# Performance work log

Measured on AMD Instinct MI355X. Metric: run time of the kernel, lower is better.

The kernel has to match this reference:

```python
import jax, jax.numpy as jnp
import numpy as np

B, C, N = 4, 256, 4096
OUT = 256
TEMP = OUT ** 0.5  # temperature = sqrt(out_channel)


def setup_inputs() -> dict:
    key = jax.random.key(0)
    kx, kxx, kq, kk, kv = jax.random.split(key, 5)
    x = jax.random.normal(kx, (B, C, N), dtype=jnp.float32)
    xx = jax.random.normal(kxx, (B, C, N), dtype=jnp.float32)
    # Conv1d(in, out, kernel=1, bias=False) weights, squeezed to (out, in)
    s = 1.0 / np.sqrt(C)
    Wq = jax.random.uniform(kq, (OUT, C), jnp.float32, -s, s)
    Wk = jax.random.uniform(kk, (OUT, C), jnp.float32, -s, s)
    Wv = jax.random.uniform(kv, (OUT, C), jnp.float32, -s, s)
    return {"x": x, "xx": xx, "Wq": Wq, "Wk": Wk, "Wv": Wv}


def reference(x, xx, Wq, Wk, Wv):
    # 1x1 conv == per-point linear: (out,in) x (b,in,n) -> (b,out,n)
    q = jnp.einsum('oc,bcn->bon', Wq, x)
    k = jnp.einsum('oc,bcn->bon', Wk, xx)
    v = jnp.einsum('oc,bcn->bon', Wv, xx)
    # attn = (q^T / temp) @ k : (B, N, N)
    attn = jax.nn.softmax(jnp.einsum('bon,bom->bnm', q, k) / TEMP, axis=-1)
    # dropout is identity in eval mode
    # y = attn @ v^T -> (B, N, OUT); returned transposed to (B, OUT, N)
    y = jnp.einsum('bnm,bom->bon', attn, v)
    return y
```

## Files before the change

kernel.cpp:

```cpp
#include <hip/hip_runtime.h>
#include <hip/hip_bf16.h>


typedef __attribute__((ext_vector_type(8))) short bf16x8;
typedef __attribute__((ext_vector_type(4))) float f32x4;
typedef __attribute__((ext_vector_type(4))) short short4t;

constexpr int B_ = 4;
constexpr int C_ = 256;
constexpr int N_ = 4096;
constexpr int O_ = 256;
constexpr float INV_TEMP = 1.0f / 16.0f;
constexpr int SPLIT = 4;
constexpr int MCHUNK = N_ / SPLIT;
constexpr int NITER = MCHUNK / 32;

__device__ __forceinline__ short f2bf(float f) {
  union { float f; unsigned u; } v; v.f = f;
  unsigned r = v.u + 0x7fffu + ((v.u >> 16) & 1u);
  return (short)(r >> 16);
}

__device__ __forceinline__ void dma16(const short* g, short* l) {
  __builtin_amdgcn_global_load_lds(
      (const __attribute__((address_space(1))) unsigned int*)g,
      (__attribute__((address_space(3))) unsigned int*)l, 16, 0, 0);
}

__global__ void wcvt(const float* __restrict__ Wq, const float* __restrict__ Wk,
                     const float* __restrict__ Wv, short* __restrict__ wb) {
  int i = blockIdx.x * 256 + threadIdx.x;
  int mat = i >> 16, off = i & 65535;
  const float* W = (mat == 0) ? Wq : (mat == 1 ? Wk : Wv);
  wb[i] = f2bf(W[off]);
}

__global__ void zero_k(float4* __restrict__ out4, float4* __restrict__ lp4) {
  int i = blockIdx.x * 256 + threadIdx.x;
  if (i < 1048576) out4[i] = (float4){0.f, 0.f, 0.f, 0.f};
  else lp4[i - 1048576] = (float4){0.f, 0.f, 0.f, 0.f};
}

__global__ void norm_k(float* __restrict__ out, const float* __restrict__ lp) {
  int i = blockIdx.x * 256 + threadIdx.x;
  int e = i * 4;
  int n = e & (N_ - 1);
  int b = e >> 20;
  float4 o = ((float4*)out)[i];
  const float4 l = *(const float4*)&lp[(b << 12) + n];
  o.x /= l.x; o.y /= l.y; o.z /= l.z; o.w /= l.w;
  ((float4*)out)[i] = o;
}

__device__ __forceinline__ void gemm64(const short* __restrict__ W,
                                       const short (*xs)[264], int w, int g,
                                       int c16, f32x4 acc[4][4]) {
#pragma unroll
  for (int i = 0; i < 4; ++i)
#pragma unroll
    for (int j = 0; j < 4; ++j) acc[i][j] = (f32x4){0.f, 0.f, 0.f, 0.f};
#pragma unroll
  for (int ko = 0; ko < 8; ++ko) {
    bf16x8 afr[4], bfr[4];
#pragma unroll
    for (int ot = 0; ot < 4; ++ot)
      afr[ot] = *(const bf16x8*)&W[(w * 64 + ot * 16 + c16) * C_ + ko * 32 + g * 8];
#pragma unroll
    for (int nt = 0; nt < 4; ++nt)
      bfr[nt] = *(const bf16x8*)&xs[nt * 16 + c16][ko * 32 + g * 8];
#pragma unroll
    for (int ot = 0; ot < 4; ++ot)
#pragma unroll
      for (int nt = 0; nt < 4; ++nt)
        acc[ot][nt] = __builtin_amdgcn_mfma_f32_16x16x32_bf16(
            afr[ot], bfr[nt], acc[ot][nt], 0, 0, 0);
  }
}

__global__ __launch_bounds__(256, 2) void qkv_proj(
    const float* __restrict__ x, const float* __restrict__ xx,
    const short* __restrict__ wb,
    short* __restrict__ qg, short* __restrict__ kt, short* __restrict__ vt) {
  const int n0  = blockIdx.x * 64;
  const int b   = blockIdx.y;
  const int mat = blockIdx.z;
  const float* src = (mat == 0) ? x : xx;
  const int tid = threadIdx.x;
  const int w = tid >> 6, lane = tid & 63;
  const int g = lane >> 4, c16 = lane & 15;

  __shared__ short xs[64][264];

  {
    const int n = tid & 63, cq = tid >> 6;
    const float* sp = src + (size_t)b * C_ * N_ + n0 + n;
#pragma unroll
    for (int rep = 0; rep < 16; ++rep) {
      int c = rep * 16 + cq * 4;
      short4t s4;
#pragma unroll
      for (int j = 0; j < 4; ++j) s4[j] = f2bf(sp[(size_t)(c + j) * N_]);
      *(short4t*)&xs[n][c] = s4;
    }
  }
  __syncthreads();

  f32x4 acc[4][4];
  if (mat == 0) {
    gemm64(wb, &xs[0], w, g, c16, acc);
    short* dst = qg + (size_t)b * N_ * O_;
#pragma unroll
    for (int ot = 0; ot < 4; ++ot)
#pragma unroll
      for (int nt = 0; nt < 4; ++nt) {
        int n = n0 + nt * 16 + c16;
        int o = w * 64 + ot * 16 + g * 4;
        short4t s;
        s[0] = f2bf(acc[ot][nt][0] * INV_TEMP);
        s[1] = f2bf(acc[ot][nt][1] * INV_TEMP);
        s[2] = f2bf(acc[ot][nt][2] * INV_TEMP);
        s[3] = f2bf(acc[ot][nt][3] * INV_TEMP);
        *(short4t*)(dst + (size_t)n * O_ + o) = s;
      }
  } else {
    gemm64(wb + 65536, &xs[0], w, g, c16, acc);
#pragma unroll
    for (int ot = 0; ot < 4; ++ot)
#pragma unroll
      for (int nt = 0; nt < 4; ++nt) {
        int m = n0 + nt * 16 + c16;
        int o0 = w * 64 + ot * 16 + g * 4;
        int koo = o0 >> 5;
        int pos = ((o0 & 31) >> 3) ^ ((c16 >> 1) & 3);
        size_t base =
            (((size_t)(b * 256 + (m >> 4)) * 8 + koo) * 16 + c16) * 32 +
            pos * 8 + (g & 1) * 4;
        short4t s;
        s[0] = f2bf(acc[ot][nt][0]);
        s[1] = f2bf(acc[ot][nt][1]);
        s[2] = f2bf(acc[ot][nt][2]);
        s[3] = f2bf(acc[ot][nt][3]);
        *(short4t*)(kt + base) = s;
      }
    gemm64(wb + 131072, &xs[0], w, g, c16, acc);
#pragma unroll
    for (int ot = 0; ot < 4; ++ot)
#pragma unroll
      for (int nt = 0; nt < 4; ++nt) {
        int m = n0 + nt * 16 + c16;
        size_t rowb = (size_t)(b * 128 + (m >> 5)) * 256;
        int gqm = (m & 31) >> 3, e = m & 7;
        int o0 = w * 64 + ot * 16 + g * 4;
#pragma unroll
        for (int r = 0; r < 4; ++r) {
          int o = o0 + r;
          int pos = gqm ^ (((o & 15) >> 1) & 3);
          vt[(rowb + o) * 32 + pos * 8 + e] = f2bf(acc[ot][nt][r]);
        }
      }
  }
}

__global__ __launch_bounds__(256, 2) void flash_attn(
    const short* __restrict__ qg, const short* __restrict__ kt,
    const short* __restrict__ vt, float* __restrict__ out,
    float* __restrict__ lp) {
  const int n0 = blockIdx.x * 128;
  const int b  = blockIdx.y;
  const int mbase = blockIdx.z * MCHUNK;
  const int tid = threadIdx.x;
  const int w = tid >> 6, lane = tid & 63;
  const int g = lane >> 4, c16 = lane & 15;

  __shared__ short kb[2][8192];
  __shared__ short vb[8192];
  __shared__ short ps[128][40];

  const short* ktb = kt + (size_t)b * N_ * O_;
  const short* vtb = vt + (size_t)b * N_ * O_;

  bf16x8 qf[2][8];
#pragma unroll
  for (int nt = 0; nt < 2; ++nt) {
    const short* qrow =
        qg + (size_t)(b * N_ + n0 + w * 32 + nt * 16 + c16) * O_ + g * 8;
#pragma unroll
    for (int ko = 0; ko < 8; ++ko) qf[nt][ko] = *(const bf16x8*)(qrow + ko * 32);
  }

  f32x4 oacc[16][2];
#pragma unroll
  for (int i = 0; i < 16; ++i)
#pragma unroll
    for (int nt = 0; nt < 2; ++nt) oacc[i][nt] = (f32x4){0.f, 0.f, 0.f, 0.f};
  float lrun[2] = {0.f, 0.f};

  {
    const short* src = ktb + (size_t)(mbase >> 4) * 4096;
#pragma unroll
    for (int j = 0; j < 4; ++j)
      dma16(src + (w * 4 + j) * 512 + lane * 8, &kb[0][(w * 4 + j) * 512]);
  }
  __syncthreads();

  const int sw = (g ^ ((c16 >> 1) & 3)) * 8;

  int cur = 0;
  for (int mi = 0; mi < NITER; ++mi) {
    {
      const short* src = vtb + ((size_t)(mbase >> 5) + mi) * 8192;
#pragma unroll
      for (int j = 0; j < 4; ++j)
        dma16(src + (w * 4 + j) * 512 + lane * 8, &vb[(w * 4 + j) * 512]);
    }
    if (mi + 1 < NITER) {
      const short* src = ktb + (size_t)((mbase >> 4) + (mi + 1) * 2) * 4096;
#pragma unroll
      for (int j = 0; j < 4; ++j)
        dma16(src + (w * 4 + j) * 512 + lane * 8, &kb[cur ^ 1][(w * 4 + j) * 512]);
    }

    f32x4 sacc[2][2];
#pragma unroll
    for (int nt = 0; nt < 2; ++nt)
#pragma unroll
      for (int t2 = 0; t2 < 2; ++t2) sacc[nt][t2] = (f32x4){0.f, 0.f, 0.f, 0.f};
#pragma unroll
    for (int ko = 0; ko < 8; ++ko) {
      const int ra = (ko * 16 + c16) * 32 + sw;
      bf16x8 kfa = *(const bf16x8*)&kb[cur][ra];
      bf16x8 kfb = *(const bf16x8*)&kb[cur][4096 + ra];
#pragma unroll
      for (int nt = 0; nt < 2; ++nt) {
        sacc[nt][0] = __builtin_amdgcn_mfma_f32_16x16x32_bf16(
            kfa, qf[nt][ko], sacc[nt][0], 0, 0, 0);
        sacc[nt][1] = __builtin_amdgcn_mfma_f32_16x16x32_bf16(
            kfb, qf[nt][ko], sacc[nt][1], 0, 0, 0);
      }
    }

#pragma unroll
    for (int nt = 0; nt < 2; ++nt) {
      float rs = 0.f;
#pragma unroll
      for (int t2 = 0; t2 < 2; ++t2) {
        short4t pb;
#pragma unroll
        for (int r = 0; r < 4; ++r) {
          float p = __expf(sacc[nt][t2][r]);
          rs += p;
          pb[r] = f2bf(p);
        }
        *(short4t*)&ps[w * 32 + nt * 16 + c16][t2 * 16 + g * 4] = pb;
      }
      rs += __shfl_xor(rs, 16);
      rs += __shfl_xor(rs, 32);
      lrun[nt] += rs;
    }

    __syncthreads();

    bf16x8 pf[2];
#pragma unroll
    for (int nt = 0; nt < 2; ++nt)
      pf[nt] = *(const bf16x8*)&ps[w * 32 + nt * 16 + c16][g * 8];
#pragma unroll
    for (int ot = 0; ot < 16; ++ot) {
      bf16x8 vf = *(const bf16x8*)&vb[(ot * 16 + c16) * 32 + sw];
#pragma unroll
      for (int nt = 0; nt < 2; ++nt)
        oacc[ot][nt] = __builtin_amdgcn_mfma_f32_16x16x32_bf16(
            vf, pf[nt], oacc[ot][nt], 0, 0, 0);
    }

    __syncthreads();
    cur ^= 1;
  }

  if (g == 0)
#pragma unroll
    for (int nt = 0; nt < 2; ++nt)
      atomicAdd(&lp[(b << 12) + n0 + w * 32 + nt * 16 + c16], lrun[nt]);

#pragma unroll
  for (int ot = 0; ot < 16; ++ot)
#pragma unroll
    for (int nt = 0; nt < 2; ++nt) {
      const int n = n0 + w * 32 + nt * 16 + c16;
      float* op = out + (size_t)b * O_ * N_ + (size_t)(ot * 16 + g * 4) * N_ + n;
#pragma unroll
      for (int r = 0; r < 4; ++r)
        atomicAdd(op + (size_t)r * N_, oacc[ot][nt][r]);
    }
}

extern "C" void kernel_launch(void* const* d_in, const int* in_sizes, int n_in,
                              void* d_out, int out_size, void* d_ws,
                              size_t ws_size, hipStream_t stream) {
  const float* x  = (const float*)d_in[0];
  const float* xx = (const float*)d_in[1];
  const float* Wq = (const float*)d_in[2];
  const float* Wk = (const float*)d_in[3];
  const float* Wv = (const float*)d_in[4];
  float* out = (float*)d_out;

  short* qg = (short*)d_ws;
  short* kt = qg + (size_t)B_ * N_ * O_;
  short* vt = kt + (size_t)B_ * N_ * O_;
  float* lp = (float*)(vt + (size_t)B_ * N_ * O_);
  short* wb = (short*)(lp + B_ * N_);

  wcvt<<<768, 256, 0, stream>>>(Wq, Wk, Wv, wb);
  zero_k<<<4112, 256, 0, stream>>>((float4*)out, (float4*)lp);
  qkv_proj<<<dim3(N_ / 64, B_, 2), 256, 0, stream>>>(x, xx, wb, qg, kt, vt);
  flash_attn<<<dim3(32, B_, SPLIT), 256, 0, stream>>>(qg, kt, vt, out, lp);
  norm_k<<<4096, 256, 0, stream>>>(out, lp);
}
```

Baseline: 219.9 us.

## Retile flash attention to 64-query blocks with 64-key steps and per-wave output slices

Reworks the attention kernel so each block handles 64 queries and 64 keys per iteration. Each wave computes scores for its own 16-key slice and owns a 64-channel slice of the output instead of all 256 channels. The key-split count drops from 4 to 2 and the grid doubles along queries, so fewer atomic partial outputs are written. The K double buffer is replaced by a single buffer whose prefetch is issued after a barrier, and V gets a new swizzled 64-wide layout written with vector stores. The projection kernel now runs Q, K and V as three separate grid slices with a transposed MFMA for V. The single K buffer can expose load latency, and the block count changes occupancy.

```diff
diff --git a/kernel.cpp b/kernel.cpp
--- a/kernel.cpp
+++ b/kernel.cpp
@@ -11,9 +11,9 @@
 constexpr int N_ = 4096;
 constexpr int O_ = 256;
 constexpr float INV_TEMP = 1.0f / 16.0f;
-constexpr int SPLIT = 4;
+constexpr int SPLIT = 2;
 constexpr int MCHUNK = N_ / SPLIT;
-constexpr int NITER = MCHUNK / 32;
+constexpr int NITER = MCHUNK / 64;
 
 __device__ __forceinline__ short f2bf(float f) {
   union { float f; unsigned u; } v; v.f = f;
@@ -52,31 +52,6 @@
   ((float4*)out)[i] = o;
 }
 
-__device__ __forceinline__ void gemm64(const short* __restrict__ W,
-                                       const short (*xs)[264], int w, int g,
-                                       int c16, f32x4 acc[4][4]) {
-#pragma unroll
-  for (int i = 0; i < 4; ++i)
-#pragma unroll
-    for (int j = 0; j < 4; ++j) acc[i][j] = (f32x4){0.f, 0.f, 0.f, 0.f};
-#pragma unroll
-  for (int ko = 0; ko < 8; ++ko) {
-    bf16x8 afr[4], bfr[4];
-#pragma unroll
-    for (int ot = 0; ot < 4; ++ot)
-      afr[ot] = *(const bf16x8*)&W[(w * 64 + ot * 16 + c16) * C_ + ko * 32 + g * 8];
-#pragma unroll
-    for (int nt = 0; nt < 4; ++nt)
-      bfr[nt] = *(const bf16x8*)&xs[nt * 16 + c16][ko * 32 + g * 8];
-#pragma unroll
-    for (int ot = 0; ot < 4; ++ot)
-#pragma unroll
-      for (int nt = 0; nt < 4; ++nt)
-        acc[ot][nt] = __builtin_amdgcn_mfma_f32_16x16x32_bf16(
-            afr[ot], bfr[nt], acc[ot][nt], 0, 0, 0);
-  }
-}
-
 __global__ __launch_bounds__(256, 2) void qkv_proj(
     const float* __restrict__ x, const float* __restrict__ xx,
     const short* __restrict__ wb,
@@ -85,6 +60,7 @@
   const int b   = blockIdx.y;
   const int mat = blockIdx.z;
   const float* src = (mat == 0) ? x : xx;
+  const short* W   = wb + mat * 65536;
   const int tid = threadIdx.x;
   const int w = tid >> 6, lane = tid & 63;
   const int g = lane >> 4, c16 = lane & 15;
@@ -106,8 +82,38 @@
   __syncthreads();
 
   f32x4 acc[4][4];
+#pragma unroll
+  for (int i = 0; i < 4; ++i)
+#pragma unroll
+    for (int j = 0; j < 4; ++j) acc[i][j] = (f32x4){0.f, 0.f, 0.f, 0.f};
+
+#pragma unroll
+  for (int ko = 0; ko < 8; ++ko) {
+    bf16x8 wfr[4], xfr[4];
+#pragma unroll
+    for (int ot = 0; ot < 4; ++ot)
+      wfr[ot] = *(const bf16x8*)&W[(w * 64 + ot * 16 + c16) * C_ + ko * 32 + g * 8];
+#pragma unroll
+    for (int nt = 0; nt < 4; ++nt)
+      xfr[nt] = *(const bf16x8*)&xs[nt * 16 + c16][ko * 32 + g * 8];
+    if (mat < 2) {
+#pragma unroll
+      for (int ot = 0; ot < 4; ++ot)
+#pragma unroll
+        for (int nt = 0; nt < 4; ++nt)
+          acc[ot][nt] = __builtin_amdgcn_mfma_f32_16x16x32_bf16(
+              wfr[ot], xfr[nt], acc[ot][nt], 0, 0, 0);
+    } else {
+#pragma unroll
+      for (int mt = 0; mt < 4; ++mt)
+#pragma unroll
+        for (int ot = 0; ot < 4; ++ot)
+          acc[mt][ot] = __builtin_amdgcn_mfma_f32_16x16x32_bf16(
+              xfr[mt], wfr[ot], acc[mt][ot], 0, 0, 0);
+    }
+  }
+
   if (mat == 0) {
-    gemm64(wb, &xs[0], w, g, c16, acc);
     short* dst = qg + (size_t)b * N_ * O_;
 #pragma unroll
     for (int ot = 0; ot < 4; ++ot)
@@ -122,8 +128,7 @@
         s[3] = f2bf(acc[ot][nt][3] * INV_TEMP);
         *(short4t*)(dst + (size_t)n * O_ + o) = s;
       }
-  } else {
-    gemm64(wb + 65536, &xs[0], w, g, c16, acc);
+  } else if (mat == 1) {
 #pragma unroll
     for (int ot = 0; ot < 4; ++ot)
 #pragma unroll
@@ -142,21 +147,23 @@
         s[3] = f2bf(acc[ot][nt][3]);
         *(short4t*)(kt + base) = s;
       }
-    gemm64(wb + 131072, &xs[0], w, g, c16, acc);
-#pragma unroll
-    for (int ot = 0; ot < 4; ++ot)
-#pragma unroll
-      for (int nt = 0; nt < 4; ++nt) {
-        int m = n0 + nt * 16 + c16;
-        size_t rowb = (size_t)(b * 128 + (m >> 5)) * 256;
-        int gqm = (m & 31) >> 3, e = m & 7;
-        int o0 = w * 64 + ot * 16 + g * 4;
-#pragma unroll
-        for (int r = 0; r < 4; ++r) {
-          int o = o0 + r;
-          int pos = gqm ^ (((o & 15) >> 1) & 3);
-          vt[(rowb + o) * 32 + pos * 8 + e] = f2bf(acc[ot][nt][r]);
-        }
+  } else {
+#pragma unroll
+    for (int mt = 0; mt < 4; ++mt)
+#pragma unroll
+      for (int ot = 0; ot < 4; ++ot) {
+        int o = w * 64 + ot * 16 + c16;
+        int mloc = mt * 16 + g * 4;
+        int chunk = mloc >> 3;
+        int pos = chunk ^ (o & 7);
+        size_t base =
+            ((size_t)(b * 64 + (n0 >> 6)) * 256 + o) * 64 + pos * 8 + (g & 1) * 4;
+        short4t s;
+        s[0] = f2bf(acc[mt][ot][0]);
+        s[1] = f2bf(acc[mt][ot][1]);
+        s[2] = f2bf(acc[mt][ot][2]);
+        s[3] = f2bf(acc[mt][ot][3]);
+        *(short4t*)(vt + base) = s;
       }
   }
 }
@@ -165,129 +172,126 @@
     const short* __restrict__ qg, const short* __restrict__ kt,
     const short* __restrict__ vt, float* __restrict__ out,
     float* __restrict__ lp) {
-  const int n0 = blockIdx.x * 128;
+  const int n0 = blockIdx.x * 64;
   const int b  = blockIdx.y;
   const int mbase = blockIdx.z * MCHUNK;
   const int tid = threadIdx.x;
   const int w = tid >> 6, lane = tid & 63;
   const int g = lane >> 4, c16 = lane & 15;
 
-  __shared__ short kb[2][8192];
-  __shared__ short vb[8192];
-  __shared__ short ps[128][40];
+  __shared__ short kb[16384];
+  __shared__ short vb[16384];
+  __shared__ short ps[64][72];
 
   const short* ktb = kt + (size_t)b * N_ * O_;
   const short* vtb = vt + (size_t)b * N_ * O_;
 
-  bf16x8 qf[2][8];
-#pragma unroll
-  for (int nt = 0; nt < 2; ++nt) {
+  bf16x8 qf[4][8];
+#pragma unroll
+  for (int nt = 0; nt < 4; ++nt) {
     const short* qrow =
-        qg + (size_t)(b * N_ + n0 + w * 32 + nt * 16 + c16) * O_ + g * 8;
+        qg + (size_t)(b * N_ + n0 + nt * 16 + c16) * O_ + g * 8;
 #pragma unroll
     for (int ko = 0; ko < 8; ++ko) qf[nt][ko] = *(const bf16x8*)(qrow + ko * 32);
   }
 
-  f32x4 oacc[16][2];
-#pragma unroll
-  for (int i = 0; i < 16; ++i)
-#pragma unroll
-    for (int nt = 0; nt < 2; ++nt) oacc[i][nt] = (f32x4){0.f, 0.f, 0.f, 0.f};
-  float lrun[2] = {0.f, 0.f};
+  f32x4 oacc[4][4];
+#pragma unroll
+  for (int i = 0; i < 4; ++i)
+#pragma unroll
+    for (int j = 0; j < 4; ++j) oacc[i][j] = (f32x4){0.f, 0.f, 0.f, 0.f};
+  float lrun[4] = {0.f, 0.f, 0.f, 0.f};
 
   {
-    const short* src = ktb + (size_t)(mbase >> 4) * 4096;
-#pragma unroll
-    for (int j = 0; j < 4; ++j)
-      dma16(src + (w * 4 + j) * 512 + lane * 8, &kb[0][(w * 4 + j) * 512]);
+    const short* src = ktb + ((size_t)(mbase >> 4) + w) * 4096;
+#pragma unroll
+    for (int j = 0; j < 8; ++j)
+      dma16(src + j * 512 + lane * 8, &kb[w * 4096 + j * 512]);
   }
   __syncthreads();
 
   const int sw = (g ^ ((c16 >> 1) & 3)) * 8;
 
-  int cur = 0;
   for (int mi = 0; mi < NITER; ++mi) {
     {
-      const short* src = vtb + ((size_t)(mbase >> 5) + mi) * 8192;
-#pragma unroll
-      for (int j = 0; j < 4; ++j)
-        dma16(src + (w * 4 + j) * 512 + lane * 8, &vb[(w * 4 + j) * 512]);
-    }
+      const short* src = vtb + ((size_t)(mbase >> 6) + mi) * 16384 + w * 4096;
+#pragma unroll
+      for (int j = 0; j < 8; ++j)
+        dma16(src + j * 512 + lane * 8, &vb[w * 4096 + j * 512]);
+    }
+
+    f32x4 sacc[4];
+#pragma unroll
+    for (int nt = 0; nt < 4; ++nt) sacc[nt] = (f32x4){0.f, 0.f, 0.f, 0.f};
+#pragma unroll
+    for (int ko = 0; ko < 8; ++ko) {
+      bf16x8 kf = *(const bf16x8*)&kb[w * 4096 + (ko * 16 + c16) * 32 + sw];
+#pragma unroll
+      for (int nt = 0; nt < 4; ++nt)
+        sacc[nt] = __builtin_amdgcn_mfma_f32_16x16x32_bf16(
+            kf, qf[nt][ko], sacc[nt], 0, 0, 0);
+    }
+
+#pragma unroll
+    for (int nt = 0; nt < 4; ++nt) {
+      short4t pb;
+      float rs = 0.f;
+#pragma unroll
+      for (int r = 0; r < 4; ++r) {
+        float p = __expf(sacc[nt][r]);
+        rs += p;
+        pb[r] = f2bf(p);
+      }
+      lrun[nt] += rs;
+      *(short4t*)&ps[nt * 16 + c16][w * 16 + g * 4] = pb;
+    }
+
+    __syncthreads();
+
     if (mi + 1 < NITER) {
-      const short* src = ktb + (size_t)((mbase >> 4) + (mi + 1) * 2) * 4096;
-#pragma unroll
-      for (int j = 0; j < 4; ++j)
-        dma16(src + (w * 4 + j) * 512 + lane * 8, &kb[cur ^ 1][(w * 4 + j) * 512]);
-    }
-
-    f32x4 sacc[2][2];
-#pragma unroll
-    for (int nt = 0; nt < 2; ++nt)
-#pragma unroll
-      for (int t2 = 0; t2 < 2; ++t2) sacc[nt][t2] = (f32x4){0.f, 0.f, 0.f, 0.f};
-#pragma unroll
-    for (int ko = 0; ko < 8; ++ko) {
-      const int ra = (ko * 16 + c16) * 32 + sw;
-      bf16x8 kfa = *(const bf16x8*)&kb[cur][ra];
-      bf16x8 kfb = *(const bf16x8*)&kb[cur][4096 + ra];
-#pragma unroll
-      for (int nt = 0; nt < 2; ++nt) {
-        sacc[nt][0] = __builtin_amdgcn_mfma_f32_16x16x32_bf16(
-            kfa, qf[nt][ko], sacc[nt][0], 0, 0, 0);
-        sacc[nt][1] = __builtin_amdgcn_mfma_f32_16x16x32_bf16(
-            kfb, qf[nt][ko], sacc[nt][1], 0, 0, 0);
-      }
-    }
-
-#pragma unroll
-    for (int nt = 0; nt < 2; ++nt) {
-      float rs = 0.f;
-#pragma unroll
-      for (int t2 = 0; t2 < 2; ++t2) {
-        short4t pb;
-#pragma unroll
-        for (int r = 0; r < 4; ++r) {
-          float p = __expf(sacc[nt][t2][r]);
-          rs += p;
-          pb[r] = f2bf(p);
-        }
-        *(short4t*)&ps[w * 32 + nt * 16 + c16][t2 * 16 + g * 4] = pb;
-      }
-      rs += __shfl_xor(rs, 16);
-      rs += __shfl_xor(rs, 32);
-      lrun[nt] += rs;
+      const short* src =
+          ktb + ((size_t)(mbase >> 4) + (mi + 1) * 4 + w) * 4096;
+#pragma unroll
+      for (int j = 0; j < 8; ++j)
+        dma16(src + j * 512 + lane * 8, &kb[w * 4096 + j * 512]);
+    }
+
+#pragma unroll
+    for (int kk = 0; kk < 2; ++kk) {
+      bf16x8 pf[4];
+#pragma unroll
+      for (int nt = 0; nt < 4; ++nt)
+        pf[nt] = *(const bf16x8*)&ps[nt * 16 + c16][kk * 32 + g * 8];
+#pragma unroll
+      for (int ot = 0; ot < 4; ++ot) {
+        int pos = (kk * 4 + g) ^ (c16 & 7);
+        bf16x8 vf =
+            *(const bf16x8*)&vb[(w * 64 + ot * 16 + c16) * 64 + pos * 8];
+#pragma unroll
+        for (int nt = 0; nt < 4; ++nt)
+          oacc[ot][nt] = __builtin_amdgcn_mfma_f32_16x16x32_bf16(
+              vf, pf[nt], oacc[ot][nt], 0, 0, 0);
+      }
     }
 
     __syncthreads();
-
-    bf16x8 pf[2];
-#pragma unroll
-    for (int nt = 0; nt < 2; ++nt)
-      pf[nt] = *(const bf16x8*)&ps[w * 32 + nt * 16 + c16][g * 8];
-#pragma unroll
-    for (int ot = 0; ot < 16; ++ot) {
-      bf16x8 vf = *(const bf16x8*)&vb[(ot * 16 + c16) * 32 + sw];
-#pragma unroll
-      for (int nt = 0; nt < 2; ++nt)
-        oacc[ot][nt] = __builtin_amdgcn_mfma_f32_16x16x32_bf16(
-            vf, pf[nt], oacc[ot][nt], 0, 0, 0);
-    }
-
-    __syncthreads();
-    cur ^= 1;
-  }
-
-  if (g == 0)
-#pragma unroll
-    for (int nt = 0; nt < 2; ++nt)
-      atomicAdd(&lp[(b << 12) + n0 + w * 32 + nt * 16 + c16], lrun[nt]);
-
-#pragma unroll
-  for (int ot = 0; ot < 16; ++ot)
-#pragma unroll
-    for (int nt = 0; nt < 2; ++nt) {
-      const int n = n0 + w * 32 + nt * 16 + c16;
-      float* op = out + (size_t)b * O_ * N_ + (size_t)(ot * 16 + g * 4) * N_ + n;
+  }
+
+#pragma unroll
+  for (int nt = 0; nt < 4; ++nt) {
+    float v = lrun[nt];
+    v += __shfl_xor(v, 16);
+    v += __shfl_xor(v, 32);
+    if (lane < 16) atomicAdd(&lp[(b << 12) + n0 + nt * 16 + lane], v);
+  }
+
+#pragma unroll
+  for (int ot = 0; ot < 4; ++ot)
+#pragma unroll
+    for (int nt = 0; nt < 4; ++nt) {
+      const int n = n0 + nt * 16 + c16;
+      float* op = out + (size_t)b * O_ * N_ +
+                  (size_t)(w * 64 + ot * 16 + g * 4) * N_ + n;
 #pragma unroll
       for (int r = 0; r < 4; ++r)
         atomicAdd(op + (size_t)r * N_, oacc[ot][nt][r]);
@@ -312,7 +316,7 @@
 
   wcvt<<<768, 256, 0, stream>>>(Wq, Wk, Wv, wb);
   zero_k<<<4112, 256, 0, stream>>>((float4*)out, (float4*)lp);
-  qkv_proj<<<dim3(N_ / 64, B_, 2), 256, 0, stream>>>(x, xx, wb, qg, kt, vt);
-  flash_attn<<<dim3(32, B_, SPLIT), 256, 0, stream>>>(qg, kt, vt, out, lp);
+  qkv_proj<<<dim3(N_ / 64, B_, 3), 256, 0, stream>>>(x, xx, wb, qg, kt, vt);
+  flash_attn<<<dim3(64, B_, SPLIT), 256, 0, stream>>>(qg, kt, vt, out, lp);
   norm_k<<<4096, 256, 0, stream>>>(out, lp);
 }
```

After: 209.2 us. 1.05x faster.
